# Kernel optimization log

Hardware: AMD Instinct MI355X
Metric: run time of the kernel (lower is better)

## Reference

```python
import jax, jax.numpy as jnp
import numpy as np

N, D = 8192, 128
TAU = 0.5
EPS = 1e-12  # F.normalize default eps


def setup_inputs() -> dict:
    key = jax.random.key(0)
    k = jax.random.split(key, 6)
    s = 1.0 / np.sqrt(D)  # torch Linear default init bound
    return {
        "z1": jax.random.normal(k[0], (N, D), dtype=jnp.float32),
        "z2": jax.random.normal(k[1], (N, D), dtype=jnp.float32),
        "w1": jax.random.uniform(k[2], (D, D), jnp.float32, -s, s),
        "b1": jax.random.uniform(k[3], (D,), jnp.float32, -s, s),
        "w2": jax.random.uniform(k[4], (D, D), jnp.float32, -s, s),
        "b2": jax.random.uniform(k[5], (D,), jnp.float32, -s, s),
    }


def _project(z, w1, b1, w2, b2):
    # fc2(elu(fc1(z))); torch Linear is x @ W.T + b
    h = jax.nn.elu(z @ w1.T + b1)
    return h @ w2.T + b2


def _normalize(z):
    n = jnp.linalg.norm(z, axis=1, keepdims=True)
    return z / jnp.maximum(n, EPS)


def _semi_loss(h1, h2):
    n1 = _normalize(h1)
    n2 = _normalize(h2)
    refl = jnp.exp((n1 @ n1.T) / TAU)   # [N, N]
    betw = jnp.exp((n1 @ n2.T) / TAU)   # [N, N]
    denom = refl.sum(axis=1) + betw.sum(axis=1) - jnp.diag(refl)
    return -jnp.log(jnp.diag(betw) / denom)


def reference(z1, z2, w1, b1, w2, b2):
    h1 = _project(z1, w1, b1, w2, b2)
    h2 = _project(z2, w1, b1, w2, b2)
    l1 = _semi_loss(h1, h2)
    l2 = _semi_loss(h2, h1)
    return ((l1 + l2) * 0.5).mean()
```

## Files before the change

kernel.cpp:

```cpp
#include <hip/hip_runtime.h>


#define NR 8192
#define DIM 128
#define SCALE_EXP2 2.885390081777927f
#define LOG2E 1.442695040888963f
#define LN2 0.6931471805599453f
#define NT 32

typedef __attribute__((ext_vector_type(8))) short short8;
typedef __attribute__((ext_vector_type(4))) float f32x4;
typedef __attribute__((ext_vector_type(16))) float f32x16;

__device__ unsigned short gN[2 * NR * DIM];
__device__ unsigned short gNs[2 * NR * DIM];
__device__ float gT[2 * NR];
__device__ float gACC;

__device__ inline float b2f(unsigned short h) {
    union { unsigned int u; float f; } x; x.u = ((unsigned int)h) << 16; return x.f;
}
__device__ inline unsigned short f2b(float f) {
    union { float f; unsigned int u; } x; x.f = f;
    return (unsigned short)((x.u + 0x7FFFu + ((x.u >> 16) & 1u)) >> 16);
}
__device__ inline short8 ldf8(const float* __restrict__ p) {
    f32x4 a = *(const f32x4*)p;
    f32x4 b = *(const f32x4*)(p + 4);
    short8 r;
#pragma unroll
    for (int j = 0; j < 4; ++j) r[j] = (short)f2b(a[j]);
#pragma unroll
    for (int j = 0; j < 4; ++j) r[4 + j] = (short)f2b(b[j]);
    return r;
}
__device__ inline f32x16 zero16() {
    f32x16 z;
#pragma unroll
    for (int i = 0; i < 16; ++i) z[i] = 0.0f;
    return z;
}
__device__ inline void gload_lds16(const void* g, void* l) {
    __builtin_amdgcn_global_load_lds(
        (const __attribute__((address_space(1))) unsigned int*)g,
        (__attribute__((address_space(3))) unsigned int*)l, 16, 0, 0);
}

__global__ __launch_bounds__(128) void k_proj(
        const float* __restrict__ Z1, const float* __restrict__ Z2,
        const float* __restrict__ W1, const float* __restrict__ B1,
        const float* __restrict__ W2, const float* __restrict__ B2) {
    __shared__ unsigned short hfrag[2][8][64][8];
    int t = threadIdx.x, w = t >> 6, l = t & 63;
    int lr = l & 31, lh = l >> 5;
    const float* Z = blockIdx.y ? Z2 : Z1;
    long rbase = (long)blockIdx.x * 64 + w * 32;

    int gi = ((int)blockIdx.y * 128 + (int)blockIdx.x) * 128 + t;
    if (gi < 2 * NR) gT[gi] = 0.0f;
    if (gi == 0) gACC = 0.0f;

    short8 zf[8];
#pragma unroll
    for (int kc = 0; kc < 8; ++kc)
        zf[kc] = ldf8(Z + (rbase + lr) * DIM + kc * 16 + lh * 8);

#pragma unroll
    for (int tt = 0; tt < 4; ++tt) {
        short8 wf[8];
#pragma unroll
        for (int kc = 0; kc < 8; ++kc)
            wf[kc] = ldf8(W1 + (tt * 32 + lr) * DIM + kc * 16 + lh * 8);
        f32x16 a = zero16();
#pragma unroll
        for (int kc = 0; kc < 8; ++kc)
            a = __builtin_amdgcn_mfma_f32_32x32x16_bf16(zf[kc], wf[kc], a, 0, 0, 0);
        float bias = B1[tt * 32 + lr];
        int col = tt * 32 + lr;
#pragma unroll
        for (int r = 0; r < 16; ++r) {
            float v = a[r] + bias;
            if (v <= 0.0f) v = __builtin_amdgcn_exp2f(v * LOG2E) - 1.0f;
            int ro = (r & 3) + 8 * (r >> 2) + 4 * lh;
            hfrag[w][col >> 4][ro | (((col >> 3) & 1) << 5)][col & 7] = f2b(v);
        }
    }
    __syncthreads();

    short8 af[8];
#pragma unroll
    for (int kc = 0; kc < 8; ++kc)
        af[kc] = *(const short8*)&hfrag[w][kc][l][0];

    f32x16 acc[4];
#pragma unroll
    for (int tt = 0; tt < 4; ++tt) {
        short8 wf[8];
#pragma unroll
        for (int kc = 0; kc < 8; ++kc)
            wf[kc] = ldf8(W2 + (tt * 32 + lr) * DIM + kc * 16 + lh * 8);
        f32x16 a = zero16();
#pragma unroll
        for (int kc = 0; kc < 8; ++kc)
            a = __builtin_amdgcn_mfma_f32_32x32x16_bf16(af[kc], wf[kc], a, 0, 0, 0);
        float bias = B2[tt * 32 + lr];
#pragma unroll
        for (int r = 0; r < 16; ++r) a[r] += bias;
        acc[tt] = a;
    }
    float ss[16];
#pragma unroll
    for (int r = 0; r < 16; ++r)
        ss[r] = acc[0][r] * acc[0][r] + acc[1][r] * acc[1][r]
              + acc[2][r] * acc[2][r] + acc[3][r] * acc[3][r];
#pragma unroll
    for (int r = 0; r < 16; ++r) {
        ss[r] += __shfl_xor(ss[r], 1);  ss[r] += __shfl_xor(ss[r], 2);
        ss[r] += __shfl_xor(ss[r], 4);  ss[r] += __shfl_xor(ss[r], 8);
        ss[r] += __shfl_xor(ss[r], 16);
    }
    long nbase = (long)blockIdx.y * NR + rbase;
#pragma unroll
    for (int r = 0; r < 16; ++r) {
        float inv = 1.0f / fmaxf(sqrtf(ss[r]), 1e-12f);
        long row = nbase + (r & 3) + 8 * (r >> 2) + 4 * lh;
#pragma unroll
        for (int tt = 0; tt < 4; ++tt) {
            float v = acc[tt][r] * inv;
            gN[row * DIM + tt * 32 + lr]  = f2b(v);
            gNs[row * DIM + tt * 32 + lr] = f2b(v * SCALE_EXP2);
        }
    }
}

__global__ __launch_bounds__(512, 4) void k_sim() {
    __shared__ char smem[2 * 16384];
    int lin = blockIdx.x;
    int slice = lin & 7, qp = lin >> 3;
    int t = threadIdx.x, w = t >> 6, l = t & 63;
    int lr = l & 31, lh = l >> 5;
    long qbase = (long)qp * 256 + w * 32;
    long kb = (long)slice * 2048;

    short8 qf[8];
#pragma unroll
    for (int kc = 0; kc < 8; ++kc)
        qf[kc] = *(const short8*)(gNs + (qbase + lr) * DIM + kc * 16 + lh * 8);
    float rs[16];
#pragma unroll
    for (int r = 0; r < 16; ++r) rs[r] = 0.0f;

#define STAGE(BUF, TILE) do {                                                        \
    const unsigned short* _tb = gN + (kb + (long)(TILE) * 64) * DIM;                 \
    int _i0 = (w << 6) | l;                                                          \
    int _j0 = (_i0 & ~15) | ((_i0 & 15) ^ ((_i0 >> 4) & 7));                         \
    gload_lds16(_tb + _j0 * 8, smem + (BUF) * 16384 + w * 1024);                     \
    int _i1 = 512 + ((w << 6) | l);                                                  \
    int _j1 = (_i1 & ~15) | ((_i1 & 15) ^ ((_i1 >> 4) & 7));                         \
    gload_lds16(_tb + _j1 * 8, smem + (BUF) * 16384 + 8192 + w * 1024);              \
} while (0)

    STAGE(0, 0);
    for (int tt = 0; tt < NT; ++tt) {
        int cur = tt & 1;
        if (tt + 1 < NT) {
            STAGE(cur ^ 1, tt + 1);
            asm volatile("s_waitcnt vmcnt(2)" ::: "memory");
        } else {
            asm volatile("s_waitcnt vmcnt(0)" ::: "memory");
        }
        __builtin_amdgcn_s_barrier();
        const char* bufp = smem + cur * 16384;
#pragma unroll
        for (int ks = 0; ks < 2; ++ks) {
            short8 bf[8];
#pragma unroll
            for (int kc = 0; kc < 8; ++kc) {
                int chunk = ((kc << 1) | lh) ^ (lr & 7);
                bf[kc] = *(const short8*)(bufp + (ks * 32 + lr) * 256 + chunk * 16);
            }
            f32x16 c = zero16();
#pragma unroll
            for (int kc = 0; kc < 8; ++kc)
                c = __builtin_amdgcn_mfma_f32_32x32x16_bf16(qf[kc], bf[kc], c, 0, 0, 0);
#pragma unroll
            for (int r = 0; r < 16; ++r)
                rs[r] += __builtin_amdgcn_exp2f(c[r]);
        }
        __builtin_amdgcn_s_barrier();
    }
#undef STAGE

#pragma unroll
    for (int r = 0; r < 16; ++r) {
        rs[r] += __shfl_xor(rs[r], 1);  rs[r] += __shfl_xor(rs[r], 2);
        rs[r] += __shfl_xor(rs[r], 4);  rs[r] += __shfl_xor(rs[r], 8);
        rs[r] += __shfl_xor(rs[r], 16);
    }
    if (lr == 0) {
#pragma unroll
        for (int r = 0; r < 16; ++r) {
            int ro = (r & 3) + 8 * (r >> 2) + 4 * lh;
            atomicAdd(&gT[qbase + ro], rs[r]);
        }
    }
}

__global__ __launch_bounds__(256) void k_loss() {
    int t = threadIdx.x, w = t >> 6, l = t & 63;
    int gw = blockIdx.x * 4 + w;
    float lsum = 0.0f;
    for (int row = gw; row < NR; row += 512) {
        unsigned int pa = *(const unsigned int*)(gN + (long)row * DIM + l * 2);
        unsigned int pb = *(const unsigned int*)(gN + (long)(NR + row) * DIM + l * 2);
        float a0 = b2f((unsigned short)(pa & 0xFFFFu)), a1 = b2f((unsigned short)(pa >> 16));
        float b0 = b2f((unsigned short)(pb & 0xFFFFu)), b1 = b2f((unsigned short)(pb >> 16));
        float sd1 = a0 * a0 + a1 * a1;
        float sd2 = b0 * b0 + b1 * b1;
        float cr  = a0 * b0 + a1 * b1;
#pragma unroll
        for (int off = 1; off < 64; off <<= 1) {
            sd1 += __shfl_xor(sd1, off);
            sd2 += __shfl_xor(sd2, off);
            cr  += __shfl_xor(cr,  off);
        }
        float d1 = gT[row]      - __builtin_amdgcn_exp2f(sd1 * SCALE_EXP2);
        float d2 = gT[NR + row] - __builtin_amdgcn_exp2f(sd2 * SCALE_EXP2);
        float v = (__builtin_amdgcn_logf(d1) + __builtin_amdgcn_logf(d2)) * LN2 - 4.0f * cr;
        if (l == 0) lsum += v;
    }
    if (l == 0) atomicAdd(&gACC, lsum * (0.5f / 8192.0f));
}

__global__ void k_final(float* __restrict__ out) {
    out[0] = gACC;
}

extern "C" void kernel_launch(void* const* d_in, const int* in_sizes, int n_in,
                              void* d_out, int out_size, void* d_ws, size_t ws_size,
                              hipStream_t stream) {
    const float* z1 = (const float*)d_in[0];
    const float* z2 = (const float*)d_in[1];
    const float* w1 = (const float*)d_in[2];
    const float* b1 = (const float*)d_in[3];
    const float* w2 = (const float*)d_in[4];
    const float* b2 = (const float*)d_in[5];

    k_proj<<<dim3(128, 2), 128, 0, stream>>>(z1, z2, w1, b1, w2, b2);
    k_sim<<<dim3(512), 512, 0, stream>>>();
    k_loss<<<dim3(128), 256, 0, stream>>>();
    k_final<<<1, 1, 0, stream>>>((float*)d_out);
}
```

Before: 120.6 us.

## Compute two query subtiles per wave in similarity kernel to reuse key fragments

Each wave in the similarity kernel now holds two 32-row query fragments and runs two MFMA chains against each key tile loaded from LDS. This doubles the work per block and halves the grid, cutting LDS reads and global key staging per query row. The projection kernel also grows to 256 threads with 128 rows per block. The cost is higher register pressure, so occupancy is lowered to 2 blocks per SIMD, and the smaller grid may underfill the GPU.

```diff
diff --git a/kernel.cpp b/kernel.cpp
--- a/kernel.cpp
+++ b/kernel.cpp
@@ -46,17 +46,17 @@
         (__attribute__((address_space(3))) unsigned int*)l, 16, 0, 0);
 }
 
-__global__ __launch_bounds__(128) void k_proj(
+__global__ __launch_bounds__(256) void k_proj(
         const float* __restrict__ Z1, const float* __restrict__ Z2,
         const float* __restrict__ W1, const float* __restrict__ B1,
         const float* __restrict__ W2, const float* __restrict__ B2) {
-    __shared__ unsigned short hfrag[2][8][64][8];
+    __shared__ unsigned short hfrag[4][8][64][8];
     int t = threadIdx.x, w = t >> 6, l = t & 63;
     int lr = l & 31, lh = l >> 5;
     const float* Z = blockIdx.y ? Z2 : Z1;
-    long rbase = (long)blockIdx.x * 64 + w * 32;
-
-    int gi = ((int)blockIdx.y * 128 + (int)blockIdx.x) * 128 + t;
+    long rbase = (long)blockIdx.x * 128 + w * 32;
+
+    int gi = ((int)blockIdx.y * 64 + (int)blockIdx.x) * 256 + t;
     if (gi < 2 * NR) gT[gi] = 0.0f;
     if (gi == 0) gACC = 0.0f;
 
@@ -133,29 +133,29 @@
     }
 }
 
-__global__ __launch_bounds__(512, 4) void k_sim() {
+__global__ __launch_bounds__(512, 2) void k_sim() {
     __shared__ char smem[2 * 16384];
-    int lin = blockIdx.x;
-    int slice = lin & 7, qp = lin >> 3;
+    int slice = blockIdx.x & 7, qp = blockIdx.x >> 3;
     int t = threadIdx.x, w = t >> 6, l = t & 63;
     int lr = l & 31, lh = l >> 5;
-    long qbase = (long)qp * 256 + w * 32;
+    long qbase = (long)qp * 512 + w * 64;
     long kb = (long)slice * 2048;
 
-    short8 qf[8];
-#pragma unroll
-    for (int kc = 0; kc < 8; ++kc)
-        qf[kc] = *(const short8*)(gNs + (qbase + lr) * DIM + kc * 16 + lh * 8);
-    float rs[16];
-#pragma unroll
-    for (int r = 0; r < 16; ++r) rs[r] = 0.0f;
+    short8 qf[2][8];
+#pragma unroll
+    for (int s = 0; s < 2; ++s)
+#pragma unroll
+        for (int kc = 0; kc < 8; ++kc)
+            qf[s][kc] = *(const short8*)(gNs + (qbase + s * 32 + lr) * DIM + kc * 16 + lh * 8);
+    float rs0[16], rs1[16];
+#pragma unroll
+    for (int r = 0; r < 16; ++r) { rs0[r] = 0.0f; rs1[r] = 0.0f; }
 
 #define STAGE(BUF, TILE) do {                                                        \
     const unsigned short* _tb = gN + (kb + (long)(TILE) * 64) * DIM;                 \
-    int _i0 = (w << 6) | l;                                                          \
-    int _j0 = (_i0 & ~15) | ((_i0 & 15) ^ ((_i0 >> 4) & 7));                         \
+    int _j0 = (t & ~15) | ((t & 15) ^ ((t >> 4) & 7));                               \
     gload_lds16(_tb + _j0 * 8, smem + (BUF) * 16384 + w * 1024);                     \
-    int _i1 = 512 + ((w << 6) | l);                                                  \
+    int _i1 = 512 + t;                                                               \
     int _j1 = (_i1 & ~15) | ((_i1 & 15) ^ ((_i1 >> 4) & 7));                         \
     gload_lds16(_tb + _j1 * 8, smem + (BUF) * 16384 + 8192 + w * 1024);              \
 } while (0)
@@ -179,13 +179,17 @@
                 int chunk = ((kc << 1) | lh) ^ (lr & 7);
                 bf[kc] = *(const short8*)(bufp + (ks * 32 + lr) * 256 + chunk * 16);
             }
-            f32x16 c = zero16();
-#pragma unroll
-            for (int kc = 0; kc < 8; ++kc)
-                c = __builtin_amdgcn_mfma_f32_32x32x16_bf16(qf[kc], bf[kc], c, 0, 0, 0);
-#pragma unroll
-            for (int r = 0; r < 16; ++r)
-                rs[r] += __builtin_amdgcn_exp2f(c[r]);
+            f32x16 c0 = zero16(), c1 = zero16();
+#pragma unroll
+            for (int kc = 0; kc < 8; ++kc) {
+                c0 = __builtin_amdgcn_mfma_f32_32x32x16_bf16(qf[0][kc], bf[kc], c0, 0, 0, 0);
+                c1 = __builtin_amdgcn_mfma_f32_32x32x16_bf16(qf[1][kc], bf[kc], c1, 0, 0, 0);
+            }
+#pragma unroll
+            for (int r = 0; r < 16; ++r) {
+                rs0[r] += __builtin_amdgcn_exp2f(c0[r]);
+                rs1[r] += __builtin_amdgcn_exp2f(c1[r]);
+            }
         }
         __builtin_amdgcn_s_barrier();
     }
@@ -193,15 +197,19 @@
 
 #pragma unroll
     for (int r = 0; r < 16; ++r) {
-        rs[r] += __shfl_xor(rs[r], 1);  rs[r] += __shfl_xor(rs[r], 2);
-        rs[r] += __shfl_xor(rs[r], 4);  rs[r] += __shfl_xor(rs[r], 8);
-        rs[r] += __shfl_xor(rs[r], 16);
+        rs0[r] += __shfl_xor(rs0[r], 1);  rs0[r] += __shfl_xor(rs0[r], 2);
+        rs0[r] += __shfl_xor(rs0[r], 4);  rs0[r] += __shfl_xor(rs0[r], 8);
+        rs0[r] += __shfl_xor(rs0[r], 16);
+        rs1[r] += __shfl_xor(rs1[r], 1);  rs1[r] += __shfl_xor(rs1[r], 2);
+        rs1[r] += __shfl_xor(rs1[r], 4);  rs1[r] += __shfl_xor(rs1[r], 8);
+        rs1[r] += __shfl_xor(rs1[r], 16);
     }
     if (lr == 0) {
 #pragma unroll
         for (int r = 0; r < 16; ++r) {
             int ro = (r & 3) + 8 * (r >> 2) + 4 * lh;
-            atomicAdd(&gT[qbase + ro], rs[r]);
+            atomicAdd(&gT[qbase + ro], rs0[r]);
+            atomicAdd(&gT[qbase + 32 + ro], rs1[r]);
         }
     }
 }
@@ -246,8 +254,8 @@
     const float* w2 = (const float*)d_in[4];
     const float* b2 = (const float*)d_in[5];
 
-    k_proj<<<dim3(128, 2), 128, 0, stream>>>(z1, z2, w1, b1, w2, b2);
-    k_sim<<<dim3(512), 512, 0, stream>>>();
+    k_proj<<<dim3(64, 2), 256, 0, stream>>>(z1, z2, w1, b1, w2, b2);
+    k_sim<<<dim3(256), 512, 0, stream>>>();
     k_loss<<<dim3(128), 256, 0, stream>>>();
     k_final<<<1, 1, 0, stream>>>((float*)d_out);
 }
```

Measured after the change: 125.6 us. 4.1% more time.
